# Kernel optimization log

Hardware: AMD Instinct MI355X
Metric: run time of the kernel (lower is better)

## Reference

```python
import jax, jax.numpy as jnp
import numpy as np

LOC_SIZE, CID_SIZE, UID_SIZE, TIM_SIZE = 10000, 300, 1000, 48
LOC_EMB, CID_EMB, UID_EMB, TIM_EMB = 256, 64, 64, 32
HID, ENC_HID = 500, 250            # hidden_size, history_hidden_size
SEQ, TGT = 2048, 256
INPUT = LOC_EMB + TIM_EMB + CID_EMB  # 352


def setup_inputs() -> dict:
    key = jax.random.key(0)
    ks = jax.random.split(key, 32)
    n = lambda i, shape, s=0.05: (jax.random.normal(ks[i], shape, dtype=jnp.float32) * s)
    d = {}
    d["loc"] = jax.random.randint(ks[0], (SEQ, 1), 0, LOC_SIZE)
    d["tim"] = jax.random.randint(ks[1], (SEQ, 1), 0, TIM_SIZE)
    d["cid"] = jax.random.randint(ks[2], (SEQ, 1), 0, CID_SIZE)
    d["uid"] = jax.random.randint(ks[3], (1,), 0, UID_SIZE)
    d["target"] = jax.random.randint(ks[4], (TGT, 1), 0, LOC_SIZE)
    d["target_len"] = TGT
    d["time_sim_matrix"] = jax.random.uniform(ks[5], (TIM_SIZE, TIM_SIZE), dtype=jnp.float32)
    # keep distances away from 0 since the model computes 1/dist
    d["poi_distance_matrix"] = jax.random.uniform(ks[6], (LOC_SIZE, LOC_SIZE), dtype=jnp.float32, minval=0.1, maxval=2.0)
    d["poi_cid_tim"] = jax.random.uniform(ks[7], (TIM_SIZE, CID_SIZE), dtype=jnp.float32)
    # embedding tables (emb_loc/emb_cid are pretrained+frozen in the original)
    d["weight"] = n(8, (LOC_SIZE, LOC_EMB))
    d["weight_cid"] = n(9, (CID_SIZE, CID_EMB))
    d["emb_uid_w"] = n(10, (UID_SIZE, UID_EMB))
    d["emb_tim_w"] = n(11, (TIM_SIZE, TIM_EMB))
    # bidirectional encoder LSTM (hidden 250), gate order i,f,g,o like torch
    d["enc_Wih_f"] = n(12, (4 * ENC_HID, INPUT))
    d["enc_Whh_f"] = n(13, (4 * ENC_HID, ENC_HID))
    d["enc_b_f"] = jnp.zeros((4 * ENC_HID,), jnp.float32)
    d["enc_Wih_b"] = n(14, (4 * ENC_HID, INPUT))
    d["enc_Whh_b"] = n(15, (4 * ENC_HID, ENC_HID))
    d["enc_b_b"] = jnp.zeros((4 * ENC_HID,), jnp.float32)
    # decoder LSTM (hidden 500)
    d["dec_Wih"] = n(16, (4 * HID, INPUT))
    d["dec_Whh"] = n(17, (4 * HID, HID))
    d["dec_b"] = jnp.zeros((4 * HID,), jnp.float32)
    # linear layers
    d["fc_user_w"] = n(18, (HID, UID_EMB))
    d["fc_user_b"] = jnp.zeros((HID,), jnp.float32)
    d["fc_final_w"] = n(19, (LOC_SIZE, 3 * HID))
    d["fc_final_b"] = jnp.zeros((LOC_SIZE,), jnp.float32)
    d["fc_final2_w"] = n(20, (HID, 3 * HID))
    d["fc_final2_b"] = jnp.zeros((HID,), jnp.float32)
    return d


def _lstm(x, Wih, Whh, b, H):
    """Single-layer LSTM, batch=1. x: [T, D] -> hs: [T, H]."""
    h0 = jnp.zeros((H,), x.dtype)
    c0 = jnp.zeros((H,), x.dtype)

    def step(carry, xt):
        h, c = carry
        z = Wih @ xt + Whh @ h + b
        i, f, g, o = jnp.split(z, 4)
        c = jax.nn.sigmoid(f) * c + jax.nn.sigmoid(i) * jnp.tanh(g)
        h = jax.nn.sigmoid(o) * jnp.tanh(c)
        return (h, c), h

    _, hs = jax.lax.scan(step, (h0, c0), x)
    return hs


def _table_attn(history, current, table, invert=False, causal=False):
    """Vectorized replacement for the nested-loop lookup attention.
    energies[i, j] = table[current[i], history[j]] (or its reciprocal),
    upper triangle left at 0 for the self-attn variants (as in the original),
    then softmax over the full row (torch F.softmax default dim=1 on 2D)."""
    e = table[current[:, None], history[None, :]]
    if invert:
        e = 1.0 / e
    if causal:
        nn_ = e.shape[0]
        e = jnp.where(jnp.tril(jnp.ones((nn_, nn_), bool)), e, jnp.zeros((), e.dtype))
    return jax.nn.softmax(e, axis=-1)


def reference(loc, tim, cid, uid, target, target_len,
              time_sim_matrix, poi_distance_matrix, poi_cid_tim,
              weight, weight_cid, emb_uid_w, emb_tim_w,
              enc_Wih_f, enc_Whh_f, enc_b_f, enc_Wih_b, enc_Whh_b, enc_b_b,
              dec_Wih, dec_Whh, dec_b,
              fc_user_w, fc_user_b, fc_final_w, fc_final_b, fc_final2_w, fc_final2_b):
    T = int(target_len)
    loc_f, tim_f, cid_f = loc[:, 0], tim[:, 0], cid[:, 0]

    # cross attention: current window attends to history via lookup tables
    attn_cid_time = _table_attn(cid_f[:-T], tim_f[-T:], poi_cid_tim)
    attn_loc = _table_attn(loc_f[:-T], loc_f[-T:], poi_distance_matrix, invert=True)
    attn_time = _table_attn(tim_f[:-T], tim_f[-T:], time_sim_matrix)
    # self attention on the current window (lower-triangular fill)
    self_cid_time = _table_attn(cid_f[-T:], tim_f[-T:], poi_cid_tim, causal=True)
    self_loc = _table_attn(loc_f[-T:], loc_f[-T:], poi_distance_matrix, invert=True, causal=True)
    self_time = _table_attn(tim_f[-T:], tim_f[-T:], time_sim_matrix, causal=True)

    # embeddings (dropout is identity in eval)
    x = jnp.concatenate([weight[loc_f], emb_tim_w[tim_f], weight_cid[cid_f]], axis=1)  # [SEQ, INPUT]
    hist_x, tgt_x = x[:-T], x[-T:]

    # bidirectional encoder over history
    hf = _lstm(hist_x, enc_Wih_f, enc_Whh_f, enc_b_f, ENC_HID)
    hb = _lstm(hist_x[::-1], enc_Wih_b, enc_Whh_b, enc_b_b, ENC_HID)[::-1]
    hidden_history = jnp.concatenate([hf, hb], axis=1)  # [SEQ-T, 2*ENC_HID=500]

    # decoder over current window
    hidden_state = _lstm(tgt_x, dec_Wih, dec_Whh, dec_b, HID)  # [T, 500]

    target_emb = weight[target[:, 0]]  # [T, LOC_EMB]

    uid_emb = emb_uid_w[uid] @ fc_user_w.T + fc_user_b  # [1, 500]
    user_attn = jax.nn.softmax(uid_emb @ hidden_history.T, axis=-1)  # [1, hist]
    context_user = user_attn @ hidden_history  # [1, 500]

    context = (attn_loc + attn_time + attn_cid_time) @ hidden_history  # [T, 500]
    hidden_state = (self_loc + self_time + self_cid_time) @ hidden_state  # [T, 500]

    hidden_state_all = hidden_state + uid_emb  # broadcast of repeat
    out = jnp.concatenate([hidden_state_all, context,
                           jnp.broadcast_to(context_user, (T, HID))], axis=1)  # [T, 1500]
    y = out @ fc_final_w.T + fc_final_b    # [T, LOC_SIZE]
    y1 = out @ fc_final2_w.T + fc_final2_b  # [T, HID]
    score = jax.nn.log_softmax(y, axis=-1)
    return score, y1, target_emb
```

## Files before the change

kernel.cpp:

```cpp
#include <hip/hip_runtime.h>
#include <stdint.h>

#define HIST 1792
#define TGT 256
#define SEQ 2048
#define INPUT 352
#define EHID 250
#define HID 500

typedef _Float16 h2_t __attribute__((ext_vector_type(2)));

static __device__ __forceinline__ float fdot2(uint32_t a, uint32_t b, float c) {
  return __builtin_amdgcn_fdot2(__builtin_bit_cast(h2_t, a),
                                __builtin_bit_cast(h2_t, b), c, false);
}
static __device__ __forceinline__ uint32_t packh2(float lo, float hi) {
  h2_t h; h[0] = (_Float16)lo; h[1] = (_Float16)hi;
  return __builtin_bit_cast(uint32_t, h);
}
static __device__ __forceinline__ uint4 packq(const float* p) {
  uint4 r;
  r.x = packh2(p[0], p[1]); r.y = packh2(p[2], p[3]);
  r.z = packh2(p[4], p[5]); r.w = packh2(p[6], p[7]);
  return r;
}
static __device__ __forceinline__ float dotq(uint4 w, uint4 h, float acc) {
  acc = fdot2(w.x, h.x, acc); acc = fdot2(w.y, h.y, acc);
  acc = fdot2(w.z, h.z, acc); acc = fdot2(w.w, h.w, acc);
  return acc;
}
static __device__ __forceinline__ float sigf(float x) {
  x = fminf(fmaxf(x, -30.f), 30.f);
  return 1.f / (1.f + __expf(-x));
}
static __device__ __forceinline__ float tanh_f(float x) {
  x = fminf(fmaxf(x, -15.f), 15.f);
  float e = __expf(2.f * x);
  return (e - 1.f) / (e + 1.f);
}

__global__ void k_embed(const int* __restrict__ loc, const int* __restrict__ tim,
                        const int* __restrict__ cid, const int* __restrict__ target,
                        const float* __restrict__ weight, const float* __restrict__ emb_tim_w,
                        const float* __restrict__ weight_cid,
                        float* __restrict__ x, float* __restrict__ te) {
  int t = blockIdx.x, tid = threadIdx.x;
  if (t < SEQ) {
    int l = loc[t], tm = tim[t], cd = cid[t];
    float* xr = x + (size_t)t * INPUT;
    for (int k = tid; k < 256; k += blockDim.x) xr[k] = weight[(size_t)l * 256 + k];
    for (int k = tid; k < 32; k += blockDim.x)  xr[256 + k] = emb_tim_w[tm * 32 + k];
    for (int k = tid; k < 64; k += blockDim.x)  xr[288 + k] = weight_cid[cd * 64 + k];
  } else {
    int i = t - SEQ;
    int tg = target[i];
    for (int k = tid; k < 256; k += blockDim.x) te[(size_t)i * 256 + k] = weight[(size_t)tg * 256 + k];
  }
}

__global__ void k_gemm_t(const float* __restrict__ A, int lda,
                         const float* __restrict__ W, const float* __restrict__ bias,
                         float* __restrict__ C, int ldc,
                         int M, int N, int K, int revA) {
  __shared__ float As[16][65];
  __shared__ float Ws[16][65];
  const int bn = blockIdx.x * 64, bm = blockIdx.y * 64;
  const int tid = threadIdx.x;
  const int tx = tid & 15, ty = tid >> 4;
  float acc[4][4] = {};
  for (int k0 = 0; k0 < K; k0 += 16) {
    for (int i = tid; i < 1024; i += 256) {
      int m = i >> 4, k = i & 15;
      int gm = bm + m, gk = k0 + k;
      float v = 0.f;
      if (gm < M && gk < K) { int am = revA ? (M - 1 - gm) : gm; v = A[(size_t)am * lda + gk]; }
      As[k][m] = v;
    }
    for (int i = tid; i < 1024; i += 256) {
      int n = i >> 4, k = i & 15;
      int gn = bn + n, gk = k0 + k;
      float v = 0.f;
      if (gn < N && gk < K) v = W[(size_t)gn * K + gk];
      Ws[k][n] = v;
    }
    __syncthreads();
#pragma unroll
    for (int k = 0; k < 16; k++) {
      float a0 = As[k][ty * 4 + 0], a1 = As[k][ty * 4 + 1], a2 = As[k][ty * 4 + 2], a3 = As[k][ty * 4 + 3];
      float b0 = Ws[k][tx * 4 + 0], b1 = Ws[k][tx * 4 + 1], b2 = Ws[k][tx * 4 + 2], b3 = Ws[k][tx * 4 + 3];
      acc[0][0] += a0 * b0; acc[0][1] += a0 * b1; acc[0][2] += a0 * b2; acc[0][3] += a0 * b3;
      acc[1][0] += a1 * b0; acc[1][1] += a1 * b1; acc[1][2] += a1 * b2; acc[1][3] += a1 * b3;
      acc[2][0] += a2 * b0; acc[2][1] += a2 * b1; acc[2][2] += a2 * b2; acc[2][3] += a2 * b3;
      acc[3][0] += a3 * b0; acc[3][1] += a3 * b1; acc[3][2] += a3 * b2; acc[3][3] += a3 * b3;
    }
    __syncthreads();
  }
  for (int i = 0; i < 4; i++) {
    int gm = bm + ty * 4 + i; if (gm >= M) continue;
    for (int j = 0; j < 4; j++) {
      int gn = bn + tx * 4 + j; if (gn >= N) continue;
      C[(size_t)gm * ldc + gn] = acc[i][j] + (bias ? bias[gn] : 0.f);
    }
  }
}

__global__ void k_gemm_nn(const float* __restrict__ A, int lda,
                          const float* __restrict__ B, int ldb,
                          const float* __restrict__ addvec,
                          float* __restrict__ C, int ldc,
                          int M, int N, int K) {
  __shared__ float As[16][65];
  __shared__ float Bs[16][65];
  const int bn = blockIdx.x * 64, bm = blockIdx.y * 64;
  const int tid = threadIdx.x;
  const int tx = tid & 15, ty = tid >> 4;
  float acc[4][4] = {};
  for (int k0 = 0; k0 < K; k0 += 16) {
    for (int i = tid; i < 1024; i += 256) {
      int m = i >> 4, k = i & 15;
      int gm = bm + m, gk = k0 + k;
      float v = 0.f;
      if (gm < M && gk < K) v = A[(size_t)gm * lda + gk];
      As[k][m] = v;
    }
    for (int i = tid; i < 1024; i += 256) {
      int k = i >> 6, n = i & 63;
      int gk = k0 + k, gn = bn + n;
      float v = 0.f;
      if (gk < K && gn < N) v = B[(size_t)gk * ldb + gn];
      Bs[k][n] = v;
    }
    __syncthreads();
#pragma unroll
    for (int k = 0; k < 16; k++) {
      float a0 = As[k][ty * 4 + 0], a1 = As[k][ty * 4 + 1], a2 = As[k][ty * 4 + 2], a3 = As[k][ty * 4 + 3];
      float b0 = Bs[k][tx * 4 + 0], b1 = Bs[k][tx * 4 + 1], b2 = Bs[k][tx * 4 + 2], b3 = Bs[k][tx * 4 + 3];
      acc[0][0] += a0 * b0; acc[0][1] += a0 * b1; acc[0][2] += a0 * b2; acc[0][3] += a0 * b3;
      acc[1][0] += a1 * b0; acc[1][1] += a1 * b1; acc[1][2] += a1 * b2; acc[1][3] += a1 * b3;
      acc[2][0] += a2 * b0; acc[2][1] += a2 * b1; acc[2][2] += a2 * b2; acc[2][3] += a2 * b3;
      acc[3][0] += a3 * b0; acc[3][1] += a3 * b1; acc[3][2] += a3 * b2; acc[3][3] += a3 * b3;
    }
    __syncthreads();
  }
  for (int i = 0; i < 4; i++) {
    int gm = bm + ty * 4 + i; if (gm >= M) continue;
    for (int j = 0; j < 4; j++) {
      int gn = bn + tx * 4 + j; if (gn >= N) continue;
      C[(size_t)gm * ldc + gn] = acc[i][j] + (addvec ? addvec[gn] : 0.f);
    }
  }
}

#define SMEM_W_BYTES (16 * 512 * 16)
__launch_bounds__(512, 1)
__global__ void k_lstm(const float* __restrict__ A_f, const float* __restrict__ A_b,
                       const float* __restrict__ A_d,
                       const float* __restrict__ Whh_f, const float* __restrict__ Whh_b,
                       const float* __restrict__ Whh_d,
                       float* __restrict__ hh, float* __restrict__ hdec,
                       float* zpub, uint32_t* hpub, int* flag_z, int* flag_h) {
  const int b = blockIdx.x;
  const int tid = threadIdx.x;
  __shared__ __align__(16) unsigned char smem[SMEM_W_BYTES + 5120];
  uint4* wl = (uint4*)smem;

  if (b < 2) {
    uint4* h4e = (uint4*)(smem + SMEM_W_BYTES);
    float* zbuf = (float*)(smem + SMEM_W_BYTES + 512);
    const float* A = (b == 0) ? A_f : A_b;
    const float* Whh = (b == 0) ? Whh_f : Whh_b;
    uint4 w0[24], w1[24];
    if (tid < 500) {
      const float* wr0 = Whh + (size_t)tid * EHID;
      const float* wr1 = Whh + (size_t)(tid + 500) * EHID;
      float tmp[32];
      for (int pass = 0; pass < 2; pass++) {
#pragma unroll
        for (int cc = 0; cc < 32; cc++) { int col = 192 + pass * 32 + cc; tmp[cc] = (col < EHID) ? wr0[col] : 0.f; }
#pragma unroll
        for (int k = 0; k < 4; k++) wl[(pass * 4 + k) * 512 + tid] = packq(tmp + 8 * k);
      }
      for (int pass = 0; pass < 2; pass++) {
#pragma unroll
        for (int cc = 0; cc < 32; cc++) { int col = 192 + pass * 32 + cc; tmp[cc] = (col < EHID) ? wr1[col] : 0.f; }
#pragma unroll
        for (int k = 0; k < 4; k++) wl[(8 + pass * 4 + k) * 512 + tid] = packq(tmp + 8 * k);
      }
#pragma unroll
      for (int q = 0; q < 24; q++) { w0[q] = packq(wr0 + 8 * q); w1[q] = packq(wr1 + 8 * q); }
    }
    if (tid < 32) h4e[tid] = make_uint4(0, 0, 0, 0);
    uint32_t* hde = (uint32_t*)h4e;
    float c = 0.f;
    __syncthreads();
    for (int t = 0; t < HIST; t++) {
      if (tid < 500) {
        float a0 = A[t * 1000 + tid];
        float a1 = A[t * 1000 + 500 + tid];
        float b0 = 0.f, b1 = 0.f;
#pragma unroll
        for (int q = 0; q < 24; q += 2) {
          uint4 h0 = h4e[q], h1 = h4e[q + 1];
          a0 = dotq(w0[q], h0, a0);
          a1 = dotq(w1[q], h0, a1);
          b0 = dotq(w0[q + 1], h1, b0);
          b1 = dotq(w1[q + 1], h1, b1);
        }
#pragma unroll
        for (int k = 0; k < 8; k += 2) {
          uint4 h0 = h4e[24 + k], h1 = h4e[25 + k];
          a0 = dotq(wl[k * 512 + tid], h0, a0);
          a1 = dotq(wl[(8 + k) * 512 + tid], h0, a1);
          b0 = dotq(wl[(k + 1) * 512 + tid], h1, b0);
          b1 = dotq(wl[(9 + k) * 512 + tid], h1, b1);
        }
        zbuf[tid] = a0 + b0;
        zbuf[500 + tid] = a1 + b1;
      }
      __syncthreads();
      float hval = 0.f;
      if (tid < EHID) {
        float zi = zbuf[tid], zf = zbuf[250 + tid], zg = zbuf[500 + tid], zo = zbuf[750 + tid];
        c = sigf(zf) * c + sigf(zi) * tanh_f(zg);
        hval = sigf(zo) * tanh_f(c);
        if (b == 0) hh[(size_t)t * HID + tid] = hval;
        else        hh[(size_t)(HIST - 1 - t) * HID + EHID + tid] = hval;
      }
      float hother = __shfl_xor(hval, 1);
      if (tid < EHID && !(tid & 1)) hde[tid >> 1] = packh2(hval, hother);
      __syncthreads();
    }
  } else {
    uint4* h4d = (uint4*)(smem + SMEM_W_BYTES);
    const int gi = b - 2;
    const int j = tid;
    const bool act = (j < 500);
    uint4 w[48];
    if (act) {
      const float* wr = Whh_d + (size_t)(gi * 500 + j) * HID;
      float tmp[32];
      for (int pass = 0; pass < 4; pass++) {
#pragma unroll
        for (int cc = 0; cc < 32; cc++) { int col = 384 + pass * 32 + cc; tmp[cc] = (col < HID) ? wr[col] : 0.f; }
#pragma unroll
        for (int k = 0; k < 4; k++) wl[(pass * 4 + k) * 512 + tid] = packq(tmp + 8 * k);
      }
#pragma unroll
      for (int q = 0; q < 48; q++) w[q] = packq(wr + 8 * q);
    }
    if (tid < 64) h4d[tid] = make_uint4(0, 0, 0, 0);
    uint32_t* hdd = (uint32_t*)h4d;
    float c = 0.f;
    __syncthreads();
    for (int t = 0; t < TGT; t++) {
      float z = 0.f;
      if (act) {
        float a0 = A_d[t * 2000 + gi * 500 + j];
        float a1 = 0.f, a2 = 0.f, a3 = 0.f;
#pragma unroll
        for (int q = 0; q < 48; q += 4) {
          uint4 h0 = h4d[q], h1 = h4d[q + 1], h2 = h4d[q + 2], h3 = h4d[q + 3];
          a0 = dotq(w[q], h0, a0);
          a1 = dotq(w[q + 1], h1, a1);
          a2 = dotq(w[q + 2], h2, a2);
          a3 = dotq(w[q + 3], h3, a3);
        }
#pragma unroll
        for (int k = 0; k < 16; k += 4) {
          uint4 h0 = h4d[48 + k], h1 = h4d[49 + k], h2 = h4d[50 + k], h3 = h4d[51 + k];
          a0 = dotq(wl[k * 512 + tid], h0, a0);
          a1 = dotq(wl[(k + 1) * 512 + tid], h1, a1);
          a2 = dotq(wl[(k + 2) * 512 + tid], h2, a2);
          a3 = dotq(wl[(k + 3) * 512 + tid], h3, a3);
        }
        z = (a0 + a1) + (a2 + a3);
      }
      if (gi < 3) {
        if (act) zpub[gi * 512 + j] = z;
        __threadfence();
        __syncthreads();
        if (tid == 0)
          __hip_atomic_store(&flag_z[t * 3 + gi], 1, __ATOMIC_RELEASE, __HIP_MEMORY_SCOPE_AGENT);
        if (tid == 0) {
          while (__hip_atomic_load(&flag_h[t], __ATOMIC_ACQUIRE, __HIP_MEMORY_SCOPE_AGENT) == 0)
            __builtin_amdgcn_s_sleep(2);
        }
        __syncthreads();
        if (tid < 250)
          hdd[tid] = __hip_atomic_load(&hpub[tid], __ATOMIC_RELAXED, __HIP_MEMORY_SCOPE_AGENT);
        __syncthreads();
      } else {
        if (tid == 0) {
          while (__hip_atomic_load(&flag_z[t * 3 + 0], __ATOMIC_ACQUIRE, __HIP_MEMORY_SCOPE_AGENT) == 0)
            __builtin_amdgcn_s_sleep(2);
          while (__hip_atomic_load(&flag_z[t * 3 + 1], __ATOMIC_ACQUIRE, __HIP_MEMORY_SCOPE_AGENT) == 0)
            __builtin_amdgcn_s_sleep(2);
          while (__hip_atomic_load(&flag_z[t * 3 + 2], __ATOMIC_ACQUIRE, __HIP_MEMORY_SCOPE_AGENT) == 0)
            __builtin_amdgcn_s_sleep(2);
        }
        __syncthreads();
        float hval = 0.f;
        if (act) {
          float zi = __hip_atomic_load(&zpub[0 * 512 + j], __ATOMIC_RELAXED, __HIP_MEMORY_SCOPE_AGENT);
          float zf = __hip_atomic_load(&zpub[1 * 512 + j], __ATOMIC_RELAXED, __HIP_MEMORY_SCOPE_AGENT);
          float zg = __hip_atomic_load(&zpub[2 * 512 + j], __ATOMIC_RELAXED, __HIP_MEMORY_SCOPE_AGENT);
          c = sigf(zf) * c + sigf(zi) * tanh_f(zg);
          hval = sigf(z) * tanh_f(c);
          hdec[(size_t)t * HID + j] = hval;
        }
        float hother = __shfl_xor(hval, 1);
        if (act && !(j & 1)) {
          uint32_t p = packh2(hval, hother);
          hdd[j >> 1] = p;
          hpub[j >> 1] = p;
        }
        __threadfence();
        __syncthreads();
        if (tid == 0)
          __hip_atomic_store(&flag_h[t], 1, __ATOMIC_RELEASE, __HIP_MEMORY_SCOPE_AGENT);
      }
    }
  }
}

__global__ void k_attn(const int* __restrict__ loc, const int* __restrict__ tim,
                       const int* __restrict__ cid,
                       const float* __restrict__ ts, const float* __restrict__ pd,
                       const float* __restrict__ pct,
                       float* __restrict__ S1, float* __restrict__ S2) {
  const int i = blockIdx.x;
  const int tid = threadIdx.x;
  __shared__ float e[HIST];
  __shared__ float red[256];
  const int loc_i = loc[HIST + i], tim_i = tim[HIST + i];
  for (int tab = 0; tab < 3; tab++) {
    for (int jj = tid; jj < HIST; jj += 256) {
      float v;
      if (tab == 0)      v = 1.f / pd[(size_t)loc_i * 10000 + loc[jj]];
      else if (tab == 1) v = ts[tim_i * 48 + tim[jj]];
      else               v = pct[tim_i * 300 + cid[jj]];
      e[jj] = v;
    }
    __syncthreads();
    float mx = -1e30f;
    for (int jj = tid; jj < HIST; jj += 256) mx = fmaxf(mx, e[jj]);
    red[tid] = mx; __syncthreads();
    for (int s = 128; s > 0; s >>= 1) { if (tid < s) red[tid] = fmaxf(red[tid], red[tid + s]); __syncthreads(); }
    mx = red[0]; __syncthreads();
    float sm = 0.f;
    for (int jj = tid; jj < HIST; jj += 256) sm += __expf(e[jj] - mx);
    red[tid] = sm; __syncthreads();
    for (int s = 128; s > 0; s >>= 1) { if (tid < s) red[tid] += red[tid + s]; __syncthreads(); }
    float inv = 1.f / red[0]; __syncthreads();
    for (int jj = tid; jj < HIST; jj += 256) {
      float p = __expf(e[jj] - mx) * inv;
      if (tab == 0) S1[(size_t)i * HIST + jj] = p; else S1[(size_t)i * HIST + jj] += p;
    }
    __syncthreads();
  }
  const int lj = loc[HIST + tid], tj = tim[HIST + tid], cj = cid[HIST + tid];
  for (int tab = 0; tab < 3; tab++) {
    float v;
    if (tab == 0)      v = 1.f / pd[(size_t)loc_i * 10000 + lj];
    else if (tab == 1) v = ts[tim_i * 48 + tj];
    else               v = pct[tim_i * 300 + cj];
    if (tid > i) v = 0.f;
    red[tid] = v; __syncthreads();
    for (int s = 128; s > 0; s >>= 1) { if (tid < s) red[tid] = fmaxf(red[tid], red[tid + s]); __syncthreads(); }
    float mx = red[0]; __syncthreads();
    float ex = __expf(v - mx);
    red[tid] = ex; __syncthreads();
    for (int s = 128; s > 0; s >>= 1) { if (tid < s) red[tid] += red[tid + s]; __syncthreads(); }
    float p = ex / red[0]; __syncthreads();
    if (tab == 0) S2[(size_t)i * TGT + tid] = p; else S2[(size_t)i * TGT + tid] += p;
    __syncthreads();
  }
}

__global__ void k_uid(const int* __restrict__ uid, const float* __restrict__ emb_uid_w,
                      const float* __restrict__ fc_user_w, const float* __restrict__ fc_user_b,
                      float* __restrict__ uid_emb) {
  const int tid = threadIdx.x;
  __shared__ float u[64];
  if (tid < 64) u[tid] = emb_uid_w[(size_t)uid[0] * 64 + tid];
  __syncthreads();
  if (tid < HID) {
    float a = fc_user_b[tid];
    for (int k = 0; k < 64; k++) a += u[k] * fc_user_w[tid * 64 + k];
    uid_emb[tid] = a;
  }
}

__global__ void k_user(const float* __restrict__ uid_emb, const float* __restrict__ hh,
                       float* __restrict__ out) {
  const int tid = threadIdx.x;
  __shared__ float s[HIST];
  __shared__ float red[1024];
  __shared__ float ue[HID];
  if (tid < HID) ue[tid] = uid_emb[tid];
  __syncthreads();
  for (int t = tid; t < HIST; t += 1024) {
    float a = 0.f;
    const float* hr = hh + (size_t)t * HID;
    for (int k = 0; k < HID; k++) a += ue[k] * hr[k];
    s[t] = a;
  }
  __syncthreads();
  float mx = -1e30f;
  for (int t = tid; t < HIST; t += 1024) mx = fmaxf(mx, s[t]);
  red[tid] = mx; __syncthreads();
  for (int st = 512; st > 0; st >>= 1) { if (tid < st) red[tid] = fmaxf(red[tid], red[tid + st]); __syncthreads(); }
  mx = red[0]; __syncthreads();
  float sm = 0.f;
  for (int t = tid; t < HIST; t += 1024) sm += __expf(s[t] - mx);
  red[tid] = sm; __syncthreads();
  for (int st = 512; st > 0; st >>= 1) { if (tid < st) red[tid] += red[tid + st]; __syncthreads(); }
  float inv = 1.f / red[0]; __syncthreads();
  for (int t = tid; t < HIST; t += 1024) s[t] = __expf(s[t] - mx) * inv;
  __syncthreads();
  if (tid < HID) {
    float a = 0.f;
    for (int t = 0; t < HIST; t++) a += s[t] * hh[(size_t)t * HID + tid];
    for (int i = 0; i < TGT; i++) out[(size_t)i * 1500 + 1000 + tid] = a;
  }
}

__global__ void k_logsoftmax(float* __restrict__ y) {
  const int i = blockIdx.x;
  const int tid = threadIdx.x;
  float* r = y + (size_t)i * 10000;
  __shared__ float red[1024];
  float mx = -1e30f;
  for (int j = tid; j < 10000; j += 1024) mx = fmaxf(mx, r[j]);
  red[tid] = mx; __syncthreads();
  for (int s = 512; s > 0; s >>= 1) { if (tid < s) red[tid] = fmaxf(red[tid], red[tid + s]); __syncthreads(); }
  mx = red[0]; __syncthreads();
  float sm = 0.f;
  for (int j = tid; j < 10000; j += 1024) sm += __expf(r[j] - mx);
  red[tid] = sm; __syncthreads();
  for (int s = 512; s > 0; s >>= 1) { if (tid < s) red[tid] += red[tid + s]; __syncthreads(); }
  float lse = mx + __logf(red[0]);
  __syncthreads();
  for (int j = tid; j < 10000; j += 1024) r[j] = r[j] - lse;
}

extern "C" void kernel_launch(void* const* d_in, const int* in_sizes, int n_in,
                              void* d_out, int out_size, void* d_ws, size_t ws_size,
                              hipStream_t stream) {
  (void)in_sizes; (void)n_in; (void)out_size; (void)ws_size;
  const int* loc = (const int*)d_in[0];
  const int* tim = (const int*)d_in[1];
  const int* cid = (const int*)d_in[2];
  const int* uid = (const int*)d_in[3];
  const int* target = (const int*)d_in[4];
  const float* ts = (const float*)d_in[6];
  const float* pd = (const float*)d_in[7];
  const float* pct = (const float*)d_in[8];
  const float* weight = (const float*)d_in[9];
  const float* weight_cid = (const float*)d_in[10];
  const float* emb_uid_w = (const float*)d_in[11];
  const float* emb_tim_w = (const float*)d_in[12];
  const float* enc_Wih_f = (const float*)d_in[13];
  const float* enc_Whh_f = (const float*)d_in[14];
  const float* enc_b_f = (const float*)d_in[15];
  const float* enc_Wih_b = (const float*)d_in[16];
  const float* enc_Whh_b = (const float*)d_in[17];
  const float* enc_b_b = (const float*)d_in[18];
  const float* dec_Wih = (const float*)d_in[19];
  const float* dec_Whh = (const float*)d_in[20];
  const float* dec_b = (const float*)d_in[21];
  const float* fc_user_w = (const float*)d_in[22];
  const float* fc_user_b = (const float*)d_in[23];
  const float* fc_final_w = (const float*)d_in[24];
  const float* fc_final_b = (const float*)d_in[25];
  const float* fc_final2_w = (const float*)d_in[26];
  const float* fc_final2_b = (const float*)d_in[27];

  float* score = (float*)d_out;
  float* y1 = score + (size_t)TGT * 10000;
  float* te = y1 + (size_t)TGT * HID;

  float* ws = (float*)d_ws;
  float* x = ws;
  float* A_f = x + (size_t)SEQ * INPUT;
  float* A_b = A_f + (size_t)HIST * 1000;
  float* A_d = A_b + (size_t)HIST * 1000;
  float* hh = A_d + (size_t)TGT * 2000;
  float* hdec = hh + (size_t)HIST * HID;
  float* S1 = hdec + (size_t)TGT * HID;
  float* S2 = S1 + (size_t)TGT * HIST;
  float* outb = S2 + (size_t)TGT * TGT;
  float* uid_emb = outb + (size_t)TGT * 1500;
  float* zpub = uid_emb + 512;
  uint32_t* hpub = (uint32_t*)(zpub + 3 * 512);
  int* flag_z = (int*)(hpub + 256);
  int* flag_h = flag_z + 3 * TGT;

  k_embed<<<dim3(SEQ + TGT), dim3(128), 0, stream>>>(loc, tim, cid, target, weight, emb_tim_w, weight_cid, x, te);

  k_gemm_t<<<dim3(16, 28), dim3(256), 0, stream>>>(x, INPUT, enc_Wih_f, enc_b_f, A_f, 1000, HIST, 1000, INPUT, 0);
  k_gemm_t<<<dim3(16, 28), dim3(256), 0, stream>>>(x, INPUT, enc_Wih_b, enc_b_b, A_b, 1000, HIST, 1000, INPUT, 1);
  k_gemm_t<<<dim3(32, 4), dim3(256), 0, stream>>>(x + (size_t)HIST * INPUT, INPUT, dec_Wih, dec_b, A_d, 2000, TGT, 2000, INPUT, 0);

  hipMemsetAsync(flag_z, 0, 4 * TGT * sizeof(int), stream);

  k_attn<<<dim3(TGT), dim3(256), 0, stream>>>(loc, tim, cid, ts, pd, pct, S1, S2);
  k_uid<<<dim3(1), dim3(512), 0, stream>>>(uid, emb_uid_w, fc_user_w, fc_user_b, uid_emb);

  k_lstm<<<dim3(6), dim3(512), 0, stream>>>(A_f, A_b, A_d, enc_Whh_f, enc_Whh_b, dec_Whh,
                                            hh, hdec, zpub, hpub, flag_z, flag_h);

  k_user<<<dim3(1), dim3(1024), 0, stream>>>(uid_emb, hh, outb);
  k_gemm_nn<<<dim3(8, 4), dim3(256), 0, stream>>>(S2, TGT, hdec, HID, uid_emb, outb, 1500, TGT, HID, TGT);
  k_gemm_nn<<<dim3(8, 4), dim3(256), 0, stream>>>(S1, HIST, hh, HID, nullptr, outb + 500, 1500, TGT, HID, HIST);

  k_gemm_t<<<dim3(157, 4), dim3(256), 0, stream>>>(outb, 1500, fc_final_w, fc_final_b, score, 10000, TGT, 10000, 1500, 0);
  k_gemm_t<<<dim3(8, 4), dim3(256), 0, stream>>>(outb, 1500, fc_final2_w, fc_final2_b, y1, 500, TGT, 500, 1500, 0);

  k_logsoftmax<<<dim3(TGT), dim3(1024), 0, stream>>>(score);
}
```

Baseline: 5.535 ms.

## Hold LSTM recurrent weights in AGPRs, double-buffer hidden state, prefetch inputs

The recurrent weight slices in the LSTM kernel are now stored mostly in accumulation registers (AGPRs), written with v_accvgpr_write and read back each step. This shrinks the shared-memory weight slice and the VGPR-resident part. The hidden-state buffer is double-buffered by step parity, and the next step's input projection is prefetched into a register during the current step. The aim is to cut LDS reads and memory latency on the sequential critical path. The cost is an extra AGPR-to-VGPR move per weight element and heavy register pressure that could cause spills.

```diff
diff --git a/kernel.cpp b/kernel.cpp
--- a/kernel.cpp
+++ b/kernel.cpp
@@ -38,6 +38,13 @@
   float e = __expf(2.f * x);
   return (e - 1.f) / (e + 1.f);
 }
+static __device__ __forceinline__ void spin_flag(volatile int* f) {
+  while (__hip_atomic_load(f, __ATOMIC_ACQUIRE, __HIP_MEMORY_SCOPE_AGENT) == 0)
+    __builtin_amdgcn_s_sleep(2);
+}
+#define AW(dst, src) asm("v_accvgpr_write_b32 %0, %1" : "=a"(dst) : "v"(src))
+#define AR(dst, src) asm("v_accvgpr_read_b32 %0, %1" : "=v"(dst) : "a"(src))
+#define ARQ(dst, arr, base) do { AR(dst.x, arr[(base)+0]); AR(dst.y, arr[(base)+1]); AR(dst.z, arr[(base)+2]); AR(dst.w, arr[(base)+3]); } while(0)
 
 __global__ void k_embed(const int* __restrict__ loc, const int* __restrict__ tim,
                         const int* __restrict__ cid, const int* __restrict__ target,
@@ -151,8 +158,9 @@
   }
 }
 
-#define SMEM_W_BYTES (16 * 512 * 16)
-__launch_bounds__(512, 1)
+#define WQL 12
+#define WBYTES (WQL * 512 * 16)
+__launch_bounds__(512)
 __global__ void k_lstm(const float* __restrict__ A_f, const float* __restrict__ A_b,
                        const float* __restrict__ A_d,
                        const float* __restrict__ Whh_f, const float* __restrict__ Whh_b,
@@ -161,61 +169,80 @@
                        float* zpub, uint32_t* hpub, int* flag_z, int* flag_h) {
   const int b = blockIdx.x;
   const int tid = threadIdx.x;
-  __shared__ __align__(16) unsigned char smem[SMEM_W_BYTES + 5120];
+  __shared__ __align__(16) unsigned char smem[WBYTES + 2048 + 4096];
   uint4* wl = (uint4*)smem;
+  uint4* hbuf = (uint4*)(smem + WBYTES);
+  float* zbuf = (float*)(smem + WBYTES + 2048);
+
+  if (tid < 128) hbuf[tid] = make_uint4(0, 0, 0, 0);
 
   if (b < 2) {
-    uint4* h4e = (uint4*)(smem + SMEM_W_BYTES);
-    float* zbuf = (float*)(smem + SMEM_W_BYTES + 512);
     const float* A = (b == 0) ? A_f : A_b;
     const float* Whh = (b == 0) ? Whh_f : Whh_b;
-    uint4 w0[24], w1[24];
-    if (tid < 500) {
+    const bool act = tid < 500;
+    uint4 wv0[10], wv1[10];
+    uint32_t wa[128];
+    if (act) {
       const float* wr0 = Whh + (size_t)tid * EHID;
       const float* wr1 = Whh + (size_t)(tid + 500) * EHID;
-      float tmp[32];
-      for (int pass = 0; pass < 2; pass++) {
-#pragma unroll
-        for (int cc = 0; cc < 32; cc++) { int col = 192 + pass * 32 + cc; tmp[cc] = (col < EHID) ? wr0[col] : 0.f; }
-#pragma unroll
-        for (int k = 0; k < 4; k++) wl[(pass * 4 + k) * 512 + tid] = packq(tmp + 8 * k);
-      }
-      for (int pass = 0; pass < 2; pass++) {
-#pragma unroll
-        for (int cc = 0; cc < 32; cc++) { int col = 192 + pass * 32 + cc; tmp[cc] = (col < EHID) ? wr1[col] : 0.f; }
-#pragma unroll
-        for (int k = 0; k < 4; k++) wl[(8 + pass * 4 + k) * 512 + tid] = packq(tmp + 8 * k);
-      }
-#pragma unroll
-      for (int q = 0; q < 24; q++) { w0[q] = packq(wr0 + 8 * q); w1[q] = packq(wr1 + 8 * q); }
-    }
-    if (tid < 32) h4e[tid] = make_uint4(0, 0, 0, 0);
-    uint32_t* hde = (uint32_t*)h4e;
+#pragma unroll
+      for (int q = 0; q < 6; q++) {
+        float t0[8], t1[8];
+#pragma unroll
+        for (int cc = 0; cc < 8; cc++) {
+          int col = 208 + 8 * q + cc;
+          t0[cc] = (col < EHID) ? wr0[col] : 0.f;
+          t1[cc] = (col < EHID) ? wr1[col] : 0.f;
+        }
+        wl[(q * 2 + 0) * 512 + tid] = packq(t0);
+        wl[(q * 2 + 1) * 512 + tid] = packq(t1);
+      }
+#pragma unroll
+      for (int k = 0; k < 16; k++) {
+        uint4 p0 = packq(wr0 + 8 * (10 + k));
+        uint4 p1 = packq(wr1 + 8 * (10 + k));
+        AW(wa[k * 4 + 0], p0.x); AW(wa[k * 4 + 1], p0.y);
+        AW(wa[k * 4 + 2], p0.z); AW(wa[k * 4 + 3], p0.w);
+        AW(wa[64 + k * 4 + 0], p1.x); AW(wa[64 + k * 4 + 1], p1.y);
+        AW(wa[64 + k * 4 + 2], p1.z); AW(wa[64 + k * 4 + 3], p1.w);
+      }
+#pragma unroll
+      for (int q = 0; q < 10; q++) { wv0[q] = packq(wr0 + 8 * q); wv1[q] = packq(wr1 + 8 * q); }
+    }
     float c = 0.f;
+    float aA = act ? A[tid] : 0.f;
+    float aB = act ? A[500 + tid] : 0.f;
     __syncthreads();
     for (int t = 0; t < HIST; t++) {
-      if (tid < 500) {
-        float a0 = A[t * 1000 + tid];
-        float a1 = A[t * 1000 + 500 + tid];
-        float b0 = 0.f, b1 = 0.f;
-#pragma unroll
-        for (int q = 0; q < 24; q += 2) {
-          uint4 h0 = h4e[q], h1 = h4e[q + 1];
-          a0 = dotq(w0[q], h0, a0);
-          a1 = dotq(w1[q], h0, a1);
-          b0 = dotq(w0[q + 1], h1, b0);
-          b1 = dotq(w1[q + 1], h1, b1);
-        }
-#pragma unroll
-        for (int k = 0; k < 8; k += 2) {
-          uint4 h0 = h4e[24 + k], h1 = h4e[25 + k];
-          a0 = dotq(wl[k * 512 + tid], h0, a0);
-          a1 = dotq(wl[(8 + k) * 512 + tid], h0, a1);
-          b0 = dotq(wl[(k + 1) * 512 + tid], h1, b0);
-          b1 = dotq(wl[(9 + k) * 512 + tid], h1, b1);
-        }
-        zbuf[tid] = a0 + b0;
-        zbuf[500 + tid] = a1 + b1;
+      const uint4* hb = hbuf + (t & 1) * 32;
+      if (act) {
+        float z0 = aA, z1 = aB, y0 = 0.f, y1 = 0.f;
+        int tn = (t + 1 < HIST) ? t + 1 : t;
+        aA = A[tn * 1000 + tid];
+        aB = A[tn * 1000 + 500 + tid];
+#pragma unroll
+        for (int q = 0; q < 10; q++) {
+          uint4 hq = hb[q];
+          z0 = dotq(wv0[q], hq, z0);
+          z1 = dotq(wv1[q], hq, z1);
+        }
+#pragma unroll
+        for (int k = 0; k < 16; k++) {
+          uint4 hq = hb[10 + k];
+          uint4 u0, u1;
+          ARQ(u0, wa, k * 4);
+          ARQ(u1, wa, 64 + k * 4);
+          y0 = dotq(u0, hq, y0);
+          y1 = dotq(u1, hq, y1);
+        }
+#pragma unroll
+        for (int q = 0; q < 6; q++) {
+          uint4 hq = hb[26 + q];
+          z0 = dotq(wl[(q * 2 + 0) * 512 + tid], hq, z0);
+          z1 = dotq(wl[(q * 2 + 1) * 512 + tid], hq, z1);
+        }
+        zbuf[tid] = z0 + y0;
+        zbuf[500 + tid] = z1 + y1;
       }
       __syncthreads();
       float hval = 0.f;
@@ -227,76 +254,86 @@
         else        hh[(size_t)(HIST - 1 - t) * HID + EHID + tid] = hval;
       }
       float hother = __shfl_xor(hval, 1);
-      if (tid < EHID && !(tid & 1)) hde[tid >> 1] = packh2(hval, hother);
+      uint32_t* hw = (uint32_t*)(hbuf + ((t + 1) & 1) * 32);
+      if (tid < EHID && !(tid & 1)) hw[tid >> 1] = packh2(hval, hother);
       __syncthreads();
     }
   } else {
-    uint4* h4d = (uint4*)(smem + SMEM_W_BYTES);
     const int gi = b - 2;
     const int j = tid;
     const bool act = (j < 500);
-    uint4 w[48];
+    uint4 wv[20];
+    uint32_t wa[128];
     if (act) {
       const float* wr = Whh_d + (size_t)(gi * 500 + j) * HID;
-      float tmp[32];
-      for (int pass = 0; pass < 4; pass++) {
-#pragma unroll
-        for (int cc = 0; cc < 32; cc++) { int col = 384 + pass * 32 + cc; tmp[cc] = (col < HID) ? wr[col] : 0.f; }
-#pragma unroll
-        for (int k = 0; k < 4; k++) wl[(pass * 4 + k) * 512 + tid] = packq(tmp + 8 * k);
-      }
-#pragma unroll
-      for (int q = 0; q < 48; q++) w[q] = packq(wr + 8 * q);
-    }
-    if (tid < 64) h4d[tid] = make_uint4(0, 0, 0, 0);
-    uint32_t* hdd = (uint32_t*)h4d;
+#pragma unroll
+      for (int q = 0; q < 12; q++) {
+        float tmp[8];
+#pragma unroll
+        for (int cc = 0; cc < 8; cc++) {
+          int col = 416 + 8 * q + cc;
+          tmp[cc] = (col < HID) ? wr[col] : 0.f;
+        }
+        wl[q * 512 + tid] = packq(tmp);
+      }
+#pragma unroll
+      for (int k = 0; k < 32; k++) {
+        uint4 pq = packq(wr + 8 * (20 + k));
+        AW(wa[k * 4 + 0], pq.x); AW(wa[k * 4 + 1], pq.y);
+        AW(wa[k * 4 + 2], pq.z); AW(wa[k * 4 + 3], pq.w);
+      }
+#pragma unroll
+      for (int q = 0; q < 20; q++) wv[q] = packq(wr + 8 * q);
+    }
+    uint32_t* hdd = (uint32_t*)hbuf;
     float c = 0.f;
+    float aD = act ? A_d[gi * 500 + j] : 0.f;
     __syncthreads();
     for (int t = 0; t < TGT; t++) {
+      const uint4* hb = hbuf + (t & 1) * 64;
       float z = 0.f;
       if (act) {
-        float a0 = A_d[t * 2000 + gi * 500 + j];
-        float a1 = 0.f, a2 = 0.f, a3 = 0.f;
-#pragma unroll
-        for (int q = 0; q < 48; q += 4) {
-          uint4 h0 = h4d[q], h1 = h4d[q + 1], h2 = h4d[q + 2], h3 = h4d[q + 3];
-          a0 = dotq(w[q], h0, a0);
-          a1 = dotq(w[q + 1], h1, a1);
-          a2 = dotq(w[q + 2], h2, a2);
-          a3 = dotq(w[q + 3], h3, a3);
-        }
-#pragma unroll
-        for (int k = 0; k < 16; k += 4) {
-          uint4 h0 = h4d[48 + k], h1 = h4d[49 + k], h2 = h4d[50 + k], h3 = h4d[51 + k];
-          a0 = dotq(wl[k * 512 + tid], h0, a0);
-          a1 = dotq(wl[(k + 1) * 512 + tid], h1, a1);
-          a2 = dotq(wl[(k + 2) * 512 + tid], h2, a2);
-          a3 = dotq(wl[(k + 3) * 512 + tid], h3, a3);
-        }
-        z = (a0 + a1) + (a2 + a3);
+        float z0 = aD, z1 = 0.f, z2 = 0.f, z3 = 0.f;
+        int tn = (t + 1 < TGT) ? t + 1 : t;
+        aD = A_d[tn * 2000 + gi * 500 + j];
+#pragma unroll
+        for (int q = 0; q < 20; q += 2) {
+          z0 = dotq(wv[q], hb[q], z0);
+          z1 = dotq(wv[q + 1], hb[q + 1], z1);
+        }
+#pragma unroll
+        for (int k = 0; k < 32; k += 2) {
+          uint4 u0, u1;
+          ARQ(u0, wa, k * 4);
+          ARQ(u1, wa, (k + 1) * 4);
+          z2 = dotq(u0, hb[20 + k], z2);
+          z3 = dotq(u1, hb[21 + k], z3);
+        }
+#pragma unroll
+        for (int q = 0; q < 12; q += 2) {
+          z0 = dotq(wl[q * 512 + tid], hb[52 + q], z0);
+          z1 = dotq(wl[(q + 1) * 512 + tid], hb[53 + q], z1);
+        }
+        z = (z0 + z1) + (z2 + z3);
       }
       if (gi < 3) {
         if (act) zpub[gi * 512 + j] = z;
         __threadfence();
         __syncthreads();
-        if (tid == 0)
+        if (tid == 0) {
           __hip_atomic_store(&flag_z[t * 3 + gi], 1, __ATOMIC_RELEASE, __HIP_MEMORY_SCOPE_AGENT);
-        if (tid == 0) {
-          while (__hip_atomic_load(&flag_h[t], __ATOMIC_ACQUIRE, __HIP_MEMORY_SCOPE_AGENT) == 0)
-            __builtin_amdgcn_s_sleep(2);
+          spin_flag(&flag_h[t]);
         }
         __syncthreads();
+        uint32_t* hw = (uint32_t*)(hbuf + ((t + 1) & 1) * 64);
         if (tid < 250)
-          hdd[tid] = __hip_atomic_load(&hpub[tid], __ATOMIC_RELAXED, __HIP_MEMORY_SCOPE_AGENT);
+          hw[tid] = __hip_atomic_load(&hpub[tid], __ATOMIC_RELAXED, __HIP_MEMORY_SCOPE_AGENT);
         __syncthreads();
       } else {
         if (tid == 0) {
-          while (__hip_atomic_load(&flag_z[t * 3 + 0], __ATOMIC_ACQUIRE, __HIP_MEMORY_SCOPE_AGENT) == 0)
-            __builtin_amdgcn_s_sleep(2);
-          while (__hip_atomic_load(&flag_z[t * 3 + 1], __ATOMIC_ACQUIRE, __HIP_MEMORY_SCOPE_AGENT) == 0)
-            __builtin_amdgcn_s_sleep(2);
-          while (__hip_atomic_load(&flag_z[t * 3 + 2], __ATOMIC_ACQUIRE, __HIP_MEMORY_SCOPE_AGENT) == 0)
-            __builtin_amdgcn_s_sleep(2);
+          spin_flag(&flag_z[t * 3 + 0]);
+          spin_flag(&flag_z[t * 3 + 1]);
+          spin_flag(&flag_z[t * 3 + 2]);
         }
         __syncthreads();
         float hval = 0.f;
@@ -309,10 +346,11 @@
           hdec[(size_t)t * HID + j] = hval;
         }
         float hother = __shfl_xor(hval, 1);
+        uint32_t* hw = (uint32_t*)(hbuf + ((t + 1) & 1) * 64);
         if (act && !(j & 1)) {
           uint32_t p = packh2(hval, hother);
-          hdd[j >> 1] = p;
-          hpub[j >> 1] = p;
+          hw[j >> 1] = p;
+          __hip_atomic_store(&hpub[j >> 1], p, __ATOMIC_RELAXED, __HIP_MEMORY_SCOPE_AGENT);
         }
         __threadfence();
         __syncthreads();
```

Measured after the change: 5.369 ms. 3.0% less time.
